# Optimization experiments

Measured on AMD Instinct MI355X. Metric: run time of the kernel, lower is better.

## Reference

```python
import jax, jax.numpy as jnp
import numpy as np

D_MODEL = 2048
NHEADS = 16
NOPE = 128
ROPE = 64
VDIM = 128
QLORA = 1536
KVLORA = 512
QHD = NOPE + ROPE  # 192
B, T = 1, 4096


def rms_norm(x, w):
    # torch.nn.RMSNorm with eps=None uses finfo(dtype).eps
    eps = jnp.finfo(x.dtype).eps
    var = jnp.mean(x * x, axis=-1, keepdims=True)
    return x * jax.lax.rsqrt(var + eps) * w


def rope_cos_sin(T, dim):
    freqs = 1.0 / (10000.0 ** (jnp.arange(0, dim, 2, dtype=jnp.float32) / dim))
    ang = jnp.arange(T, dtype=jnp.float32)[:, None] * freqs[None, :]  # (T, dim/2)
    return jnp.cos(ang), jnp.sin(ang)


def apply_rope(x, cos, sin):
    # interleaved RoPE: even/odd channel pairs rotated
    xe = x[..., 0::2]
    xo = x[..., 1::2]
    re = xe * cos - xo * sin
    ro = xo * cos + xe * sin
    return jnp.stack([re, ro], axis=-1).reshape(x.shape)


def setup_inputs() -> dict:
    key = jax.random.key(0)
    ks = jax.random.split(key, 6)
    s = 0.02
    return {
        "x": jax.random.normal(ks[0], (B, T, D_MODEL), jnp.float32),
        "Wqa": jax.random.normal(ks[1], (D_MODEL, QLORA), jnp.float32) * s,
        "q_ln_w": jnp.ones((QLORA,), jnp.float32),
        "Wqb": jax.random.normal(ks[2], (QLORA, NHEADS * QHD), jnp.float32) * s,
        "Wkva": jax.random.normal(ks[3], (D_MODEL, KVLORA + ROPE), jnp.float32) * s,
        "kv_ln_w": jnp.ones((KVLORA,), jnp.float32),
        "Wkvb": jax.random.normal(ks[4], (KVLORA, NHEADS * (NOPE + VDIM)), jnp.float32) * s,
        "Wo": jax.random.normal(ks[5], (NHEADS * VDIM, D_MODEL), jnp.float32) * s,
    }


def reference(x, Wqa, q_ln_w, Wqb, Wkva, kv_ln_w, Wkvb, Wo):
    Bx, Tx, _ = x.shape
    cos, sin = rope_cos_sin(Tx, ROPE)  # (T, ROPE/2)

    # Low-rank Q path
    q = rms_norm(x @ Wqa, q_ln_w) @ Wqb
    q = q.reshape(Bx, Tx, NHEADS, QHD).transpose(0, 2, 1, 3)  # (B,H,T,QHD)
    q_nope = q[..., :NOPE]
    q_rope = apply_rope(q[..., NOPE:], cos, sin)  # (B,H,T,ROPE)

    # Compressed KV path + shared rope key
    kv = x @ Wkva
    kv_c = kv[..., :KVLORA]  # (B,T,KVLORA) latent cache
    k_rope = apply_rope(kv[..., KVLORA:], cos, sin)  # (B,T,ROPE), head-shared

    kvb = (rms_norm(kv_c, kv_ln_w) @ Wkvb).reshape(Bx, Tx, NHEADS, NOPE + VDIM)
    k_nope = kvb[..., :NOPE].transpose(0, 2, 1, 3)  # (B,H,T,NOPE)
    v = kvb[..., NOPE:].transpose(0, 2, 1, 3)       # (B,H,T,VDIM)

    # Scores split into nope part + head-shared rope part (avoids expanding k_rope to H heads)
    scale = 1.0 / jnp.sqrt(jnp.float32(QHD))
    s = jnp.einsum('bhqd,bhkd->bhqk', q_nope, k_nope)
    s = s + jnp.einsum('bhqd,bkd->bhqk', q_rope, k_rope)
    s = s * scale

    mask = jnp.tril(jnp.ones((Tx, Tx), dtype=bool))
    s = jnp.where(mask, s, -jnp.inf)
    a = jax.nn.softmax(s, axis=-1)

    o = jnp.einsum('bhqk,bhkd->bhqd', a, v)
    o = o.transpose(0, 2, 1, 3).reshape(Bx, Tx, NHEADS * VDIM)
    return o @ Wo
```

## Files before the change

### kernel.cpp

```cpp
#include <hip/hip_runtime.h>
#include <hip/hip_bf16.h>

typedef __attribute__((ext_vector_type(8))) short short8;
typedef __attribute__((ext_vector_type(4))) float f32x4;

#define GLDS16(gp, lp)                                                         \
  __builtin_amdgcn_global_load_lds(                                            \
      (const __attribute__((address_space(1))) void*)(gp),                     \
      (__attribute__((address_space(3))) void*)(lp), 16, 0, 0)

static __device__ __forceinline__ unsigned int pack_bf16(float a, float b) {
  __hip_bfloat16 ba = __float2bfloat16(a), bb = __float2bfloat16(b);
  unsigned short ua = *reinterpret_cast<unsigned short*>(&ba);
  unsigned short ub = *reinterpret_cast<unsigned short*>(&bb);
  return (unsigned int)ua | ((unsigned int)ub << 16);
}

__global__ __launch_bounds__(256) void cast_bf16_kernel(
    const float* __restrict__ in, __hip_bfloat16* __restrict__ out, int n4)
{
  int i = blockIdx.x * 256 + threadIdx.x;
  if (i < n4) {
    float4 v = ((const float4*)in)[i];
    out[(size_t)i * 4 + 0] = __float2bfloat16(v.x);
    out[(size_t)i * 4 + 1] = __float2bfloat16(v.y);
    out[(size_t)i * 4 + 2] = __float2bfloat16(v.z);
    out[(size_t)i * 4 + 3] = __float2bfloat16(v.w);
  }
}

__global__ void transpose_cast_kernel(const float* __restrict__ in,
                                      __hip_bfloat16* __restrict__ out,
                                      int K, int N, int Npad)
{
  __shared__ float tile[32][33];
  int n0 = blockIdx.x * 32, k0 = blockIdx.y * 32;
  int tx = threadIdx.x, ty = threadIdx.y;
  #pragma unroll
  for (int i = ty; i < 32; i += 8) {
    int k = k0 + i, n = n0 + tx;
    tile[i][tx] = (n < N) ? in[(size_t)k * N + n] : 0.f;
  }
  __syncthreads();
  #pragma unroll
  for (int i = ty; i < 32; i += 8) {
    int n = n0 + i, k = k0 + tx;
    if (n < Npad) out[(size_t)n * K + k] = __float2bfloat16(tile[tx][i]);
  }
}

__global__ __launch_bounds__(256) void gemm_bt_kernel(
    const __hip_bfloat16* __restrict__ A,
    const __hip_bfloat16* __restrict__ BT,
    float* __restrict__ C, int M, int N, int K)
{
  __shared__ __hip_bfloat16 As[128 * 32];
  __shared__ __hip_bfloat16 Bs[128 * 32];
  const int tid = threadIdx.x;
  const int wave = tid >> 6, lane = tid & 63;
  const int wr = wave >> 1, wc = wave & 1;
  const int lq = lane & 15, grp = lane >> 4;
  const int row0 = blockIdx.y * 128, col0 = blockIdx.x * 128;

  const f32x4 z4 = {0.f, 0.f, 0.f, 0.f};
  f32x4 acc[4][4];
  #pragma unroll
  for (int i = 0; i < 4; i++)
    #pragma unroll
    for (int j = 0; j < 4; j++) acc[i][j] = z4;

  for (int k0 = 0; k0 < K; k0 += 32) {
    #pragma unroll
    for (int i = 0; i < 2; i++) {
      const int t = wave + 4 * i;
      const int c = t * 64 + lane;
      const int cr = c >> 2;
      const int ko = (c & 3) << 3;
      GLDS16(A + (size_t)(row0 + cr) * K + (k0 + ko), (char*)As + t * 1024);
      GLDS16(BT + (size_t)(col0 + cr) * K + (k0 + ko), (char*)Bs + t * 1024);
    }
    __syncthreads();
    short8 af[4], bfr[4];
    #pragma unroll
    for (int mm = 0; mm < 4; mm++)
      af[mm] = *(const short8*)((const short*)As + ((wr * 64 + mm * 16 + lq) * 32 + grp * 8));
    #pragma unroll
    for (int nn = 0; nn < 4; nn++)
      bfr[nn] = *(const short8*)((const short*)Bs + ((wc * 64 + nn * 16 + lq) * 32 + grp * 8));
    #pragma unroll
    for (int mm = 0; mm < 4; mm++)
      #pragma unroll
      for (int nn = 0; nn < 4; nn++)
        acc[mm][nn] = __builtin_amdgcn_mfma_f32_16x16x32_bf16(af[mm], bfr[nn], acc[mm][nn], 0, 0, 0);
    __syncthreads();
  }
  #pragma unroll
  for (int mm = 0; mm < 4; mm++)
    #pragma unroll
    for (int nn = 0; nn < 4; nn++) {
      const int row = row0 + wr * 64 + mm * 16 + grp * 4;
      const int col = col0 + wc * 64 + nn * 16 + lq;
      float* Cp = C + (size_t)row * N + col;
      #pragma unroll
      for (int rr = 0; rr < 4; rr++) Cp[(size_t)rr * N] = acc[mm][nn][rr];
    }
}

__global__ __launch_bounds__(256) void rmsnorm_cast_kernel(
    const float* __restrict__ in, int ld_in, const float* __restrict__ w,
    __hip_bfloat16* __restrict__ out, int W)
{
  const int row = blockIdx.x;
  const int tid = threadIdx.x;
  const int wave = tid >> 6, lane = tid & 63;
  const float* x = in + (size_t)row * ld_in;
  float ss = 0.f;
  for (int i = tid; i < W; i += 256) { float v = x[i]; ss += v * v; }
  #pragma unroll
  for (int o = 32; o; o >>= 1) ss += __shfl_xor(ss, o);
  __shared__ float red[4];
  __shared__ float stot;
  if (lane == 0) red[wave] = ss;
  __syncthreads();
  if (tid == 0) stot = red[0] + red[1] + red[2] + red[3];
  __syncthreads();
  const float rstd = rsqrtf(stot / (float)W + 1.1920929e-7f);
  for (int i = tid; i < W; i += 256)
    out[(size_t)row * W + i] = __float2bfloat16(x[i] * rstd * w[i]);
}

__global__ void rope_k_kernel(const float* __restrict__ kv, __hip_bfloat16* __restrict__ kr)
{
  int t = blockIdx.x;
  int i = threadIdx.x;
  if (i < 32) {
    float freq = powf(10000.f, -2.f * (float)i / 64.f);
    float ang = (float)t * freq;
    float c = cosf(ang), s = sinf(ang);
    float xe = kv[(size_t)t * 640 + 512 + 2 * i];
    float xo = kv[(size_t)t * 640 + 512 + 2 * i + 1];
    kr[(size_t)t * 64 + 2 * i]     = __float2bfloat16(xe * c - xo * s);
    kr[(size_t)t * 64 + 2 * i + 1] = __float2bfloat16(xo * c + xe * s);
  }
}

__global__ __launch_bounds__(256) void prep_q_kernel(const float* __restrict__ q,
                                                     __hip_bfloat16* __restrict__ Qh)
{
  const int t = blockIdx.x;
  const int tid = threadIdx.x;
  __shared__ float cs[32], sn[32];
  if (tid < 32) {
    float freq = powf(10000.f, -2.f * (float)tid / 64.f);
    float ang = (float)t * freq;
    cs[tid] = cosf(ang);
    sn[tid] = sinf(ang);
  }
  __syncthreads();
  const float scale = 0.10411654209f;
  const float* qt = q + (size_t)t * 3072;
  for (int e = tid; e < 2048; e += 256) {
    int h = e >> 7, d = e & 127;
    Qh[((size_t)h * 4096 + t) * 192 + d] = __float2bfloat16(qt[h * 192 + d] * scale);
  }
  for (int e = tid; e < 512; e += 256) {
    int h = e >> 5, i = e & 31;
    float xe = qt[h * 192 + 128 + 2 * i];
    float xo = qt[h * 192 + 128 + 2 * i + 1];
    float re = xe * cs[i] - xo * sn[i];
    float ro = xo * cs[i] + xe * sn[i];
    size_t base = ((size_t)h * 4096 + t) * 192 + 128 + 2 * i;
    Qh[base]     = __float2bfloat16(re * scale);
    Qh[base + 1] = __float2bfloat16(ro * scale);
  }
}

__global__ __launch_bounds__(256) void prep_k_kernel(const float* __restrict__ kvb,
                                                     const __hip_bfloat16* __restrict__ kr,
                                                     __hip_bfloat16* __restrict__ Kh)
{
  const int t = blockIdx.x;
  const int tid = threadIdx.x;
  const float* bt = kvb + (size_t)t * 4096;
  for (int e = tid; e < 2048; e += 256) {
    int h = e >> 7, d = e & 127;
    Kh[((size_t)h * 4096 + t) * 192 + d] = __float2bfloat16(bt[h * 256 + d]);
  }
  for (int e = tid; e < 1024; e += 256) {
    int h = e >> 6, d = e & 63;
    Kh[((size_t)h * 4096 + t) * 192 + 128 + d] = kr[(size_t)t * 64 + d];
  }
}

__global__ void prep_v_kernel(const float* __restrict__ kvb, __hip_bfloat16* __restrict__ Vt)
{
  __shared__ float tile[32][33];
  int h = blockIdx.z;
  int t0 = blockIdx.y * 32, v0 = blockIdx.x * 32;
  int tx = threadIdx.x, ty = threadIdx.y;
  #pragma unroll
  for (int i = ty; i < 32; i += 8)
    tile[i][tx] = kvb[(size_t)(t0 + i) * 4096 + h * 256 + 128 + v0 + tx];
  __syncthreads();
  #pragma unroll
  for (int i = ty; i < 32; i += 8)
    Vt[((size_t)h * 128 + v0 + i) * 4096 + t0 + tx] = __float2bfloat16(tile[tx][i]);
}

__global__ __launch_bounds__(256, 2) void flash_attn_kernel(
    const __hip_bfloat16* __restrict__ Qh,
    const __hip_bfloat16* __restrict__ Kh,
    const __hip_bfloat16* __restrict__ Vt,
    __hip_bfloat16* __restrict__ Obf)
{
  __shared__ __align__(16) char Klds[2][24576];
  __shared__ __align__(16) char Vlds[2][16384];

  const int h = blockIdx.y;
  const int wave = threadIdx.x >> 6;
  const int lane = threadIdx.x & 63;
  const int lq = lane & 15;
  const int grp = lane >> 4;
  const int p = blockIdx.x;
  const int qb_[2] = {(63 - p) * 64 + wave * 16,
                      p * 64 + wave * 16};
  const int kendA = qb_[0] + 16;
  const int kendB = qb_[1] + 16;
  const int nt = 64 - p;

  const char* Kh_ = (const char*)(Kh + (size_t)h * 4096 * 192);
  const char* Vh_ = (const char*)(Vt + (size_t)h * 128 * 4096);
  const short* Qh_ = (const short*)Qh + (size_t)h * 4096 * 192;

  int kbase[6], vbase[4];
  #pragma unroll
  for (int i = 0; i < 6; i++) {
    int L = (wave * 6 + i) * 1024 + lane * 16;
    int r = L / 384, c = L - r * 384;
    int swb = (r & 3) | (((r >> 3) & 1) << 2);
    kbase[i] = r * 384 + (c ^ (swb << 4));
  }
  #pragma unroll
  for (int i = 0; i < 4; i++) {
    int L = (wave * 4 + i) * 1024 + lane * 16;
    int r = L >> 7, c = L & 127;
    vbase[i] = r * 8192 + (c ^ ((r & 7) << 4));
  }

  short8 qf[2][6];
  #pragma unroll
  for (int f = 0; f < 2; f++)
    #pragma unroll
    for (int d = 0; d < 6; d++)
      qf[f][d] = *(const short8*)(Qh_ + (size_t)(qb_[f] + lq) * 192 + d * 32 + grp * 8);

  const f32x4 z4 = {0.f, 0.f, 0.f, 0.f};
  f32x4 o_acc[2][8];
  #pragma unroll
  for (int f = 0; f < 2; f++)
    #pragma unroll
    for (int v = 0; v < 8; v++) o_acc[f][v] = z4;
  float m[2] = {-1e30f, -1e30f};
  float lsum[2] = {0.f, 0.f};

  const int krow_l = ((lq >> 2) << 3) + (lq & 3);
  const int kxm = ((lq & 3) | (((lq >> 2) & 1) << 2)) << 4;
  const int vxm = (lq & 7) << 4;

  {
    #pragma unroll
    for (int i = 0; i < 6; i++) GLDS16(Kh_ + kbase[i], Klds[0] + (wave * 6 + i) * 1024);
    #pragma unroll
    for (int i = 0; i < 4; i++) GLDS16(Vh_ + vbase[i], Vlds[0] + (wave * 4 + i) * 1024);
  }

  for (int t = 0; t < nt; t++) {
    __syncthreads();
    if (t + 1 < nt) {
      const char* Kp = Kh_ + (size_t)(t + 1) * 64 * 384;
      const char* Vp = Vh_ + (size_t)(t + 1) * 128;
      char* Kd = Klds[(t + 1) & 1];
      char* Vd = Vlds[(t + 1) & 1];
      #pragma unroll
      for (int i = 0; i < 6; i++) GLDS16(Kp + kbase[i], Kd + (wave * 6 + i) * 1024);
      #pragma unroll
      for (int i = 0; i < 4; i++) GLDS16(Vp + vbase[i], Vd + (wave * 4 + i) * 1024);
    }
    const char* Kb = Klds[t & 1];
    const char* Vb = Vlds[t & 1];
    const int ks = t * 64;

    #pragma unroll
    for (int h2 = 0; h2 < 2; h2++) {
      const int ks32 = ks + h2 * 32;
      if (ks32 >= kendA) continue;
      const bool act1 = (ks32 < kendB);

      f32x4 st[2][2];
      #pragma unroll
      for (int kt = 0; kt < 2; kt++) {
        const int row = h2 * 32 + krow_l + kt * 4;
        short8 kf[6];
        #pragma unroll
        for (int d = 0; d < 6; d++)
          kf[d] = *(const short8*)(Kb + row * 384 + ((d * 64 + grp * 16) ^ kxm));
        #pragma unroll
        for (int f = 0; f < 2; f++) {
          if (f == 1 && !act1) continue;
          f32x4 acc = z4;
          #pragma unroll
          for (int d = 0; d < 6; d++)
            acc = __builtin_amdgcn_mfma_f32_16x16x32_bf16(kf[d], qf[f][d], acc, 0, 0, 0);
          st[f][kt] = acc;
        }
      }

      short8 vf[8];
      #pragma unroll
      for (int v = 0; v < 8; v++)
        vf[v] = *(const short8*)(Vb + (v * 16 + lq) * 128 + ((h2 * 64 + grp * 16) ^ vxm));

      #pragma unroll
      for (int f = 0; f < 2; f++) {
        if (f == 1 && !act1) continue;
        const int qg = qb_[f] + lq;
        const bool need_mask = (ks32 + 31 > qb_[f]);
        if (need_mask) {
          #pragma unroll
          for (int kt = 0; kt < 2; kt++)
            #pragma unroll
            for (int r = 0; r < 4; r++) {
              int key = ks32 + grp * 8 + kt * 4 + r;
              if (key > qg) st[f][kt][r] = -1e30f;
            }
        }
        float tmax = fmaxf(fmaxf(fmaxf(st[f][0][0], st[f][0][1]), fmaxf(st[f][0][2], st[f][0][3])),
                           fmaxf(fmaxf(st[f][1][0], st[f][1][1]), fmaxf(st[f][1][2], st[f][1][3])));
        tmax = fmaxf(tmax, __shfl_xor(tmax, 16));
        tmax = fmaxf(tmax, __shfl_xor(tmax, 32));
        if (!__all(tmax <= m[f] + 11.5416f)) {
          float mnew = fmaxf(m[f], tmax);
          float alpha = exp2f(m[f] - mnew);
          m[f] = mnew;
          lsum[f] *= alpha;
          float a0 = __shfl(alpha, grp * 4 + 0);
          float a1 = __shfl(alpha, grp * 4 + 1);
          float a2 = __shfl(alpha, grp * 4 + 2);
          float a3 = __shfl(alpha, grp * 4 + 3);
          #pragma unroll
          for (int v = 0; v < 8; v++) {
            o_acc[f][v][0] *= a0; o_acc[f][v][1] *= a1;
            o_acc[f][v][2] *= a2; o_acc[f][v][3] *= a3;
          }
        }
        float p00 = exp2f(st[f][0][0] - m[f]), p01 = exp2f(st[f][0][1] - m[f]);
        float p02 = exp2f(st[f][0][2] - m[f]), p03 = exp2f(st[f][0][3] - m[f]);
        float p10 = exp2f(st[f][1][0] - m[f]), p11 = exp2f(st[f][1][1] - m[f]);
        float p12 = exp2f(st[f][1][2] - m[f]), p13 = exp2f(st[f][1][3] - m[f]);
        float psum = ((p00 + p01) + (p02 + p03)) + ((p10 + p11) + (p12 + p13));
        psum += __shfl_xor(psum, 16);
        psum += __shfl_xor(psum, 32);
        lsum[f] += psum;
        union { unsigned int u[4]; short8 s8; } pu;
        pu.u[0] = pack_bf16(p00, p01);
        pu.u[1] = pack_bf16(p02, p03);
        pu.u[2] = pack_bf16(p10, p11);
        pu.u[3] = pack_bf16(p12, p13);
        short8 pa = pu.s8;
        #pragma unroll
        for (int v = 0; v < 8; v++)
          o_acc[f][v] = __builtin_amdgcn_mfma_f32_16x16x32_bf16(pa, vf[v], o_acc[f][v], 0, 0, 0);
      }
    }
  }

  #pragma unroll
  for (int f = 0; f < 2; f++) {
    float linv = 1.f / lsum[f];
    float l0 = __shfl(linv, grp * 4 + 0);
    float l1 = __shfl(linv, grp * 4 + 1);
    float l2 = __shfl(linv, grp * 4 + 2);
    float l3 = __shfl(linv, grp * 4 + 3);
    const int qb = qb_[f];
    #pragma unroll
    for (int v = 0; v < 8; v++) {
      int col = h * 128 + v * 16 + lq;
      Obf[(size_t)(qb + grp * 4 + 0) * 2048 + col] = __float2bfloat16(o_acc[f][v][0] * l0);
      Obf[(size_t)(qb + grp * 4 + 1) * 2048 + col] = __float2bfloat16(o_acc[f][v][1] * l1);
      Obf[(size_t)(qb + grp * 4 + 2) * 2048 + col] = __float2bfloat16(o_acc[f][v][2] * l2);
      Obf[(size_t)(qb + grp * 4 + 3) * 2048 + col] = __float2bfloat16(o_acc[f][v][3] * l3);
    }
  }
}

extern "C" void kernel_launch(void* const* d_in, const int* in_sizes, int n_in,
                              void* d_out, int out_size, void* d_ws, size_t ws_size,
                              hipStream_t stream)
{
  (void)in_sizes; (void)n_in; (void)out_size; (void)ws_size;
  const float* x     = (const float*)d_in[0];
  const float* Wqa   = (const float*)d_in[1];
  const float* qlnw  = (const float*)d_in[2];
  const float* Wqb   = (const float*)d_in[3];
  const float* Wkva  = (const float*)d_in[4];
  const float* kvlnw = (const float*)d_in[5];
  const float* Wkvb  = (const float*)d_in[6];
  const float* Wo    = (const float*)d_in[7];
  float* out = (float*)d_out;
  char* ws = (char*)d_ws;

  size_t off = 0;
  auto take = [&](size_t bytes) {
    char* p = ws + off;
    off += (bytes + 255) & ~(size_t)255;
    return p;
  };

  __hip_bfloat16* x_bf  = (__hip_bfloat16*)take((size_t)4096 * 2048 * 2);
  __hip_bfloat16* WqaT  = (__hip_bfloat16*)take((size_t)1536 * 2048 * 2);
  __hip_bfloat16* WqbT  = (__hip_bfloat16*)take((size_t)3072 * 1536 * 2);
  __hip_bfloat16* WkvaT = (__hip_bfloat16*)take((size_t)640 * 2048 * 2);
  __hip_bfloat16* WkvbT = (__hip_bfloat16*)take((size_t)4096 * 512 * 2);
  __hip_bfloat16* WoT   = (__hip_bfloat16*)take((size_t)2048 * 2048 * 2);
  char* regA            = take((size_t)4096 * 1536 * 4);
  float* kv             = (float*)take((size_t)4096 * 640 * 4);
  __hip_bfloat16* q_ln  = (__hip_bfloat16*)take((size_t)4096 * 1536 * 2);
  __hip_bfloat16* kv_ln = (__hip_bfloat16*)take((size_t)4096 * 512 * 2);
  __hip_bfloat16* kr    = (__hip_bfloat16*)take((size_t)4096 * 64 * 2);
  char* regB            = take((size_t)4096 * 3072 * 4);
  char* regC            = take((size_t)4096 * 4096 * 4);

  float* q_lat = (float*)regA;
  __hip_bfloat16* Qh = (__hip_bfloat16*)regA;
  float* q_f32 = (float*)regB;
  __hip_bfloat16* Khp = (__hip_bfloat16*)regB;
  __hip_bfloat16* Vtp = (__hip_bfloat16*)(regB + (size_t)16 * 4096 * 192 * 2);
  float* kvb = (float*)regC;
  __hip_bfloat16* o_bf = (__hip_bfloat16*)regC;

  cast_bf16_kernel<<<dim3(8192), 256, 0, stream>>>(x, x_bf, 2097152);
  transpose_cast_kernel<<<dim3(48, 64), dim3(32, 8), 0, stream>>>(Wqa, WqaT, 2048, 1536, 1536);
  transpose_cast_kernel<<<dim3(96, 48), dim3(32, 8), 0, stream>>>(Wqb, WqbT, 1536, 3072, 3072);
  transpose_cast_kernel<<<dim3(20, 64), dim3(32, 8), 0, stream>>>(Wkva, WkvaT, 2048, 576, 640);
  transpose_cast_kernel<<<dim3(128, 16), dim3(32, 8), 0, stream>>>(Wkvb, WkvbT, 512, 4096, 4096);
  transpose_cast_kernel<<<dim3(64, 64), dim3(32, 8), 0, stream>>>(Wo, WoT, 2048, 2048, 2048);

  gemm_bt_kernel<<<dim3(12, 32), 256, 0, stream>>>(x_bf, WqaT, q_lat, 4096, 1536, 2048);
  gemm_bt_kernel<<<dim3(5, 32), 256, 0, stream>>>(x_bf, WkvaT, kv, 4096, 640, 2048);

  rmsnorm_cast_kernel<<<dim3(4096), 256, 0, stream>>>(q_lat, 1536, qlnw, q_ln, 1536);
  rmsnorm_cast_kernel<<<dim3(4096), 256, 0, stream>>>(kv, 640, kvlnw, kv_ln, 512);
  rope_k_kernel<<<dim3(4096), 64, 0, stream>>>(kv, kr);

  gemm_bt_kernel<<<dim3(24, 32), 256, 0, stream>>>(q_ln, WqbT, q_f32, 4096, 3072, 1536);
  prep_q_kernel<<<dim3(4096), 256, 0, stream>>>(q_f32, Qh);
  gemm_bt_kernel<<<dim3(32, 32), 256, 0, stream>>>(kv_ln, WkvbT, kvb, 4096, 4096, 512);
  prep_k_kernel<<<dim3(4096), 256, 0, stream>>>(kvb, kr, Khp);
  prep_v_kernel<<<dim3(4, 128, 16), dim3(32, 8), 0, stream>>>(kvb, Vtp);

  flash_attn_kernel<<<dim3(32, 16), 256, 0, stream>>>(Qh, Khp, Vtp, o_bf);

  gemm_bt_kernel<<<dim3(16, 32), 256, 0, stream>>>(o_bf, WoT, out, 4096, 2048, 2048);
}
```

Measured before the change: 525.2 us.

## Fuse Q/KV up-projection epilogues with RoPE and head layout, swizzle blocks across XCDs

The Q up-projection GEMM now applies RoPE and the softmax scale in its epilogue and writes bf16 straight into the per-head Q layout, using a precomputed cos/sin table. The KV up-projection GEMM writes K-nope and the transposed V directly. This removes the fp32 intermediates and the separate prep_q/prep_k/prep_v passes. GEMM blocks are remapped so neighbouring tiles land on the same XCD, and flash attention uses a 1D grid that interleaves heads for better L2 locality. The risk is that the epilogue stores are scattered, uncoalesced 2-byte writes.

Result: faster. 510.1 us (-2.9%).

```diff
diff --git a/kernel.cpp b/kernel.cpp
--- a/kernel.cpp
+++ b/kernel.cpp
@@ -14,6 +14,10 @@
   unsigned short ua = *reinterpret_cast<unsigned short*>(&ba);
   unsigned short ub = *reinterpret_cast<unsigned short*>(&bb);
   return (unsigned int)ua | ((unsigned int)ub << 16);
+}
+
+static __device__ __forceinline__ int xcd_swz(int linear, int nwg) {
+  return (linear & 7) * (nwg >> 3) + (linear >> 3);
 }
 
 __global__ __launch_bounds__(256) void cast_bf16_kernel(
@@ -49,51 +53,57 @@
   }
 }
 
+__global__ void rope_tab_kernel(float* __restrict__ cs, float* __restrict__ sn)
+{
+  int t = blockIdx.x, i = threadIdx.x;
+  float freq = powf(10000.f, -2.f * (float)i / 64.f);
+  float ang = (float)t * freq;
+  cs[t * 32 + i] = cosf(ang);
+  sn[t * 32 + i] = sinf(ang);
+}
+
+#define GEMM_MAIN(A, BT, Kdim)                                                 \
+  __shared__ __hip_bfloat16 As[128 * 32];                                      \
+  __shared__ __hip_bfloat16 Bs[128 * 32];                                      \
+  const int tid = threadIdx.x;                                                 \
+  const int wave = tid >> 6, lane = tid & 63;                                  \
+  const int wr = wave >> 1, wc = wave & 1;                                     \
+  const int lq = lane & 15, grp = lane >> 4;                                   \
+  const int nwg = gridDim.x * gridDim.y;                                       \
+  const int orig = xcd_swz(blockIdx.y * gridDim.x + blockIdx.x, nwg);          \
+  const int row0 = (orig / gridDim.x) * 128;                                   \
+  const int col0 = (orig % gridDim.x) * 128;                                   \
+  const f32x4 z4 = {0.f, 0.f, 0.f, 0.f};                                       \
+  f32x4 acc[4][4];                                                             \
+  _Pragma("unroll") for (int i = 0; i < 4; i++)                                \
+      _Pragma("unroll") for (int j = 0; j < 4; j++) acc[i][j] = z4;            \
+  for (int k0 = 0; k0 < (Kdim); k0 += 32) {                                    \
+    _Pragma("unroll") for (int i = 0; i < 2; i++) {                            \
+      const int t = wave + 4 * i;                                              \
+      const int c = t * 64 + lane;                                             \
+      const int cr = c >> 2;                                                   \
+      const int ko = (c & 3) << 3;                                             \
+      GLDS16((A) + (size_t)(row0 + cr) * (Kdim) + (k0 + ko), (char*)As + t * 1024); \
+      GLDS16((BT) + (size_t)(col0 + cr) * (Kdim) + (k0 + ko), (char*)Bs + t * 1024);\
+    }                                                                          \
+    __syncthreads();                                                           \
+    short8 af[4], bfr[4];                                                      \
+    _Pragma("unroll") for (int mm = 0; mm < 4; mm++)                           \
+      af[mm] = *(const short8*)((const short*)As + ((wr * 64 + mm * 16 + lq) * 32 + grp * 8)); \
+    _Pragma("unroll") for (int nn = 0; nn < 4; nn++)                           \
+      bfr[nn] = *(const short8*)((const short*)Bs + ((wc * 64 + nn * 16 + lq) * 32 + grp * 8));\
+    _Pragma("unroll") for (int mm = 0; mm < 4; mm++)                           \
+      _Pragma("unroll") for (int nn = 0; nn < 4; nn++)                         \
+        acc[mm][nn] = __builtin_amdgcn_mfma_f32_16x16x32_bf16(af[mm], bfr[nn], acc[mm][nn], 0, 0, 0); \
+    __syncthreads();                                                           \
+  }
+
 __global__ __launch_bounds__(256) void gemm_bt_kernel(
     const __hip_bfloat16* __restrict__ A,
     const __hip_bfloat16* __restrict__ BT,
     float* __restrict__ C, int M, int N, int K)
 {
-  __shared__ __hip_bfloat16 As[128 * 32];
-  __shared__ __hip_bfloat16 Bs[128 * 32];
-  const int tid = threadIdx.x;
-  const int wave = tid >> 6, lane = tid & 63;
-  const int wr = wave >> 1, wc = wave & 1;
-  const int lq = lane & 15, grp = lane >> 4;
-  const int row0 = blockIdx.y * 128, col0 = blockIdx.x * 128;
-
-  const f32x4 z4 = {0.f, 0.f, 0.f, 0.f};
-  f32x4 acc[4][4];
-  #pragma unroll
-  for (int i = 0; i < 4; i++)
-    #pragma unroll
-    for (int j = 0; j < 4; j++) acc[i][j] = z4;
-
-  for (int k0 = 0; k0 < K; k0 += 32) {
-    #pragma unroll
-    for (int i = 0; i < 2; i++) {
-      const int t = wave + 4 * i;
-      const int c = t * 64 + lane;
-      const int cr = c >> 2;
-      const int ko = (c & 3) << 3;
-      GLDS16(A + (size_t)(row0 + cr) * K + (k0 + ko), (char*)As + t * 1024);
-      GLDS16(BT + (size_t)(col0 + cr) * K + (k0 + ko), (char*)Bs + t * 1024);
-    }
-    __syncthreads();
-    short8 af[4], bfr[4];
-    #pragma unroll
-    for (int mm = 0; mm < 4; mm++)
-      af[mm] = *(const short8*)((const short*)As + ((wr * 64 + mm * 16 + lq) * 32 + grp * 8));
-    #pragma unroll
-    for (int nn = 0; nn < 4; nn++)
-      bfr[nn] = *(const short8*)((const short*)Bs + ((wc * 64 + nn * 16 + lq) * 32 + grp * 8));
-    #pragma unroll
-    for (int mm = 0; mm < 4; mm++)
-      #pragma unroll
-      for (int nn = 0; nn < 4; nn++)
-        acc[mm][nn] = __builtin_amdgcn_mfma_f32_16x16x32_bf16(af[mm], bfr[nn], acc[mm][nn], 0, 0, 0);
-    __syncthreads();
-  }
+  GEMM_MAIN(A, BT, K)
   #pragma unroll
   for (int mm = 0; mm < 4; mm++)
     #pragma unroll
@@ -103,6 +113,71 @@
       float* Cp = C + (size_t)row * N + col;
       #pragma unroll
       for (int rr = 0; rr < 4; rr++) Cp[(size_t)rr * N] = acc[mm][nn][rr];
+    }
+}
+
+__global__ __launch_bounds__(256) void gemm_qup_kernel(
+    const __hip_bfloat16* __restrict__ A,
+    const __hip_bfloat16* __restrict__ BT,
+    __hip_bfloat16* __restrict__ Qh,
+    const float* __restrict__ cs_tab, const float* __restrict__ sn_tab, int K)
+{
+  GEMM_MAIN(A, BT, K)
+  const float scale = 0.10411654209f;
+  #pragma unroll
+  for (int mm = 0; mm < 4; mm++)
+    #pragma unroll
+    for (int nn = 0; nn < 4; nn++) {
+      const int col = col0 + wc * 64 + nn * 16 + lq;
+      const int h = col / 192;
+      const int d = col - h * 192;
+      const bool is_rope = (d >= 128);
+      const int i = (d - 128) >> 1;
+      const float sgn = (d & 1) ? 1.f : -1.f;
+      #pragma unroll
+      for (int rr = 0; rr < 4; rr++) {
+        const int t = row0 + wr * 64 + mm * 16 + grp * 4 + rr;
+        float val = acc[mm][nn][rr];
+        float partner = __shfl_xor(val, 1);
+        float outv = val;
+        if (is_rope) {
+          float c = cs_tab[t * 32 + i];
+          float s = sn_tab[t * 32 + i];
+          outv = val * c + sgn * partner * s;
+        }
+        Qh[((size_t)h * 4096 + t) * 192 + d] = __float2bfloat16(outv * scale);
+      }
+    }
+}
+
+__global__ __launch_bounds__(256) void gemm_kvup_kernel(
+    const __hip_bfloat16* __restrict__ A,
+    const __hip_bfloat16* __restrict__ BT,
+    __hip_bfloat16* __restrict__ Kh,
+    __hip_bfloat16* __restrict__ Vt, int K)
+{
+  GEMM_MAIN(A, BT, K)
+  #pragma unroll
+  for (int mm = 0; mm < 4; mm++)
+    #pragma unroll
+    for (int nn = 0; nn < 4; nn++) {
+      const int col = col0 + wc * 64 + nn * 16 + lq;
+      const int h = col >> 8;
+      const int j = col & 255;
+      if (j < 128) {
+        #pragma unroll
+        for (int rr = 0; rr < 4; rr++) {
+          const int t = row0 + wr * 64 + mm * 16 + grp * 4 + rr;
+          Kh[((size_t)h * 4096 + t) * 192 + j] = __float2bfloat16(acc[mm][nn][rr]);
+        }
+      } else {
+        const int vd = j - 128;
+        const int t0 = row0 + wr * 64 + mm * 16 + grp * 4;
+        uint2 w;
+        w.x = pack_bf16(acc[mm][nn][0], acc[mm][nn][1]);
+        w.y = pack_bf16(acc[mm][nn][2], acc[mm][nn][3]);
+        *(uint2*)(Vt + ((size_t)h * 128 + vd) * 4096 + t0) = w;
+      }
     }
 }
 
@@ -144,67 +219,15 @@
   }
 }
 
-__global__ __launch_bounds__(256) void prep_q_kernel(const float* __restrict__ q,
-                                                     __hip_bfloat16* __restrict__ Qh)
+__global__ __launch_bounds__(256) void prep_krope_kernel(
+    const __hip_bfloat16* __restrict__ kr, __hip_bfloat16* __restrict__ Kh)
 {
   const int t = blockIdx.x;
   const int tid = threadIdx.x;
-  __shared__ float cs[32], sn[32];
-  if (tid < 32) {
-    float freq = powf(10000.f, -2.f * (float)tid / 64.f);
-    float ang = (float)t * freq;
-    cs[tid] = cosf(ang);
-    sn[tid] = sinf(ang);
-  }
-  __syncthreads();
-  const float scale = 0.10411654209f;
-  const float* qt = q + (size_t)t * 3072;
-  for (int e = tid; e < 2048; e += 256) {
-    int h = e >> 7, d = e & 127;
-    Qh[((size_t)h * 4096 + t) * 192 + d] = __float2bfloat16(qt[h * 192 + d] * scale);
-  }
-  for (int e = tid; e < 512; e += 256) {
-    int h = e >> 5, i = e & 31;
-    float xe = qt[h * 192 + 128 + 2 * i];
-    float xo = qt[h * 192 + 128 + 2 * i + 1];
-    float re = xe * cs[i] - xo * sn[i];
-    float ro = xo * cs[i] + xe * sn[i];
-    size_t base = ((size_t)h * 4096 + t) * 192 + 128 + 2 * i;
-    Qh[base]     = __float2bfloat16(re * scale);
-    Qh[base + 1] = __float2bfloat16(ro * scale);
-  }
-}
-
-__global__ __launch_bounds__(256) void prep_k_kernel(const float* __restrict__ kvb,
-                                                     const __hip_bfloat16* __restrict__ kr,
-                                                     __hip_bfloat16* __restrict__ Kh)
-{
-  const int t = blockIdx.x;
-  const int tid = threadIdx.x;
-  const float* bt = kvb + (size_t)t * 4096;
-  for (int e = tid; e < 2048; e += 256) {
-    int h = e >> 7, d = e & 127;
-    Kh[((size_t)h * 4096 + t) * 192 + d] = __float2bfloat16(bt[h * 256 + d]);
-  }
   for (int e = tid; e < 1024; e += 256) {
     int h = e >> 6, d = e & 63;
     Kh[((size_t)h * 4096 + t) * 192 + 128 + d] = kr[(size_t)t * 64 + d];
   }
-}
-
-__global__ void prep_v_kernel(const float* __restrict__ kvb, __hip_bfloat16* __restrict__ Vt)
-{
-  __shared__ float tile[32][33];
-  int h = blockIdx.z;
-  int t0 = blockIdx.y * 32, v0 = blockIdx.x * 32;
-  int tx = threadIdx.x, ty = threadIdx.y;
-  #pragma unroll
-  for (int i = ty; i < 32; i += 8)
-    tile[i][tx] = kvb[(size_t)(t0 + i) * 4096 + h * 256 + 128 + v0 + tx];
-  __syncthreads();
-  #pragma unroll
-  for (int i = ty; i < 32; i += 8)
-    Vt[((size_t)h * 128 + v0 + i) * 4096 + t0 + tx] = __float2bfloat16(tile[tx][i]);
 }
 
 __global__ __launch_bounds__(256, 2) void flash_attn_kernel(
@@ -216,12 +239,15 @@
   __shared__ __align__(16) char Klds[2][24576];
   __shared__ __align__(16) char Vlds[2][16384];
 
-  const int h = blockIdx.y;
+  const int hw = blockIdx.x;
+  const int rest = hw >> 3;
+  const int h = (hw & 7) + 8 * (rest & 1);
+  const int p = rest >> 1;
+
   const int wave = threadIdx.x >> 6;
   const int lane = threadIdx.x & 63;
   const int lq = lane & 15;
   const int grp = lane >> 4;
-  const int p = blockIdx.x;
   const int qb_[2] = {(63 - p) * 64 + wave * 16,
                       p * 64 + wave * 16};
   const int kendA = qb_[0] + 16;
@@ -427,16 +453,14 @@
   __hip_bfloat16* q_ln  = (__hip_bfloat16*)take((size_t)4096 * 1536 * 2);
   __hip_bfloat16* kv_ln = (__hip_bfloat16*)take((size_t)4096 * 512 * 2);
   __hip_bfloat16* kr    = (__hip_bfloat16*)take((size_t)4096 * 64 * 2);
-  char* regB            = take((size_t)4096 * 3072 * 4);
-  char* regC            = take((size_t)4096 * 4096 * 4);
+  float* cs_tab         = (float*)take((size_t)4096 * 32 * 4);
+  float* sn_tab         = (float*)take((size_t)4096 * 32 * 4);
+  __hip_bfloat16* Khp   = (__hip_bfloat16*)take((size_t)16 * 4096 * 192 * 2);
+  __hip_bfloat16* Vtp   = (__hip_bfloat16*)take((size_t)16 * 128 * 4096 * 2);
+  __hip_bfloat16* o_bf  = (__hip_bfloat16*)take((size_t)4096 * 2048 * 2);
 
   float* q_lat = (float*)regA;
   __hip_bfloat16* Qh = (__hip_bfloat16*)regA;
-  float* q_f32 = (float*)regB;
-  __hip_bfloat16* Khp = (__hip_bfloat16*)regB;
-  __hip_bfloat16* Vtp = (__hip_bfloat16*)(regB + (size_t)16 * 4096 * 192 * 2);
-  float* kvb = (float*)regC;
-  __hip_bfloat16* o_bf = (__hip_bfloat16*)regC;
 
   cast_bf16_kernel<<<dim3(8192), 256, 0, stream>>>(x, x_bf, 2097152);
   transpose_cast_kernel<<<dim3(48, 64), dim3(32, 8), 0, stream>>>(Wqa, WqaT, 2048, 1536, 1536);
@@ -444,6 +468,7 @@
   transpose_cast_kernel<<<dim3(20, 64), dim3(32, 8), 0, stream>>>(Wkva, WkvaT, 2048, 576, 640);
   transpose_cast_kernel<<<dim3(128, 16), dim3(32, 8), 0, stream>>>(Wkvb, WkvbT, 512, 4096, 4096);
   transpose_cast_kernel<<<dim3(64, 64), dim3(32, 8), 0, stream>>>(Wo, WoT, 2048, 2048, 2048);
+  rope_tab_kernel<<<dim3(4096), 32, 0, stream>>>(cs_tab, sn_tab);
 
   gemm_bt_kernel<<<dim3(12, 32), 256, 0, stream>>>(x_bf, WqaT, q_lat, 4096, 1536, 2048);
   gemm_bt_kernel<<<dim3(5, 32), 256, 0, stream>>>(x_bf, WkvaT, kv, 4096, 640, 2048);
@@ -452,13 +477,11 @@
   rmsnorm_cast_kernel<<<dim3(4096), 256, 0, stream>>>(kv, 640, kvlnw, kv_ln, 512);
   rope_k_kernel<<<dim3(4096), 64, 0, stream>>>(kv, kr);
 
-  gemm_bt_kernel<<<dim3(24, 32), 256, 0, stream>>>(q_ln, WqbT, q_f32, 4096, 3072, 1536);
-  prep_q_kernel<<<dim3(4096), 256, 0, stream>>>(q_f32, Qh);
-  gemm_bt_kernel<<<dim3(32, 32), 256, 0, stream>>>(kv_ln, WkvbT, kvb, 4096, 4096, 512);
-  prep_k_kernel<<<dim3(4096), 256, 0, stream>>>(kvb, kr, Khp);
-  prep_v_kernel<<<dim3(4, 128, 16), dim3(32, 8), 0, stream>>>(kvb, Vtp);
-
-  flash_attn_kernel<<<dim3(32, 16), 256, 0, stream>>>(Qh, Khp, Vtp, o_bf);
+  gemm_qup_kernel<<<dim3(24, 32), 256, 0, stream>>>(q_ln, WqbT, Qh, cs_tab, sn_tab, 1536);
+  gemm_kvup_kernel<<<dim3(32, 32), 256, 0, stream>>>(kv_ln, WkvbT, Khp, Vtp, 512);
+  prep_krope_kernel<<<dim3(4096), 256, 0, stream>>>(kr, Khp);
+
+  flash_attn_kernel<<<dim3(512), 256, 0, stream>>>(Qh, Khp, Vtp, o_bf);
 
   gemm_bt_kernel<<<dim3(16, 32), 256, 0, stream>>>(o_bf, WoT, out, 4096, 2048, 2048);
 }
```
